# Performance work log

Measured on AMD Instinct MI355X. Metric: run time of the kernel, lower is better.

Reference implementation:

```python
import jax, jax.numpy as jnp
import numpy as np

DECAY = 0.99
EPS = 1e-06


def setup_inputs() -> dict:
    key = jax.random.key(0)
    k1, k2, k3 = jax.random.split(key, 3)
    B, S, D, K = 8, 8192, 256, 2048
    x = jax.random.normal(k1, (B, S, D), dtype=jnp.float32)
    embed = jax.random.normal(k2, (K, D), dtype=jnp.float32)
    cluster_size = jnp.ones((K,), dtype=jnp.float32)
    embed_avg = jax.random.normal(k3, (K, D), dtype=jnp.float32)
    return {"x": x, "embed": embed, "cluster_size": cluster_size, "embed_avg": embed_avg}


def reference(x, embed, cluster_size, embed_avg):
    # x: [B, S, D]; embed/embed_avg: [K, D]; cluster_size: [K]
    B, S, D = x.shape
    K = embed.shape[0]
    xf = x.reshape(-1, D)  # [N, D]
    dist = (
        jnp.sum(xf * xf, axis=1, keepdims=True)
        - 2.0 * (xf @ embed.T)
        + jnp.sum(embed * embed, axis=1)
    )
    embed_ind_flat = jnp.argmin(dist, axis=-1)  # [N]
    quantize = embed[embed_ind_flat].reshape(B, S, D)
    embed_ind = embed_ind_flat.reshape(B, S)

    # EMA updates (training branch). one_hot.sum(0) == per-code counts,
    # one_hot.T @ x == per-code feature sums; use segment_sum (no NxK one-hot).
    counts = jax.ops.segment_sum(
        jnp.ones((B * S,), dtype=jnp.float32), embed_ind_flat, num_segments=K
    )
    embed_sum = jax.ops.segment_sum(xf, embed_ind_flat, num_segments=K)  # [K, D]
    new_cluster_size = cluster_size * DECAY + (1.0 - DECAY) * counts
    new_embed_avg = embed_avg * DECAY + (1.0 - DECAY) * embed_sum
    total = new_cluster_size.sum()
    smoothed = (new_cluster_size + EPS) / (total + EPS * K) * total  # laplace smoothing
    new_embed = new_embed_avg / smoothed[:, None]
    return quantize, embed_ind, new_cluster_size, new_embed_avg, new_embed
```

## Files before the change

kernel.cpp:

```cpp
#include <hip/hip_runtime.h>
#include <hip/hip_fp16.h>
#include <float.h>

#define DECAY 0.99f
#define OMD   0.01f
#define EPSF  1e-6f

constexpr int Bb = 8, Ss = 8192, Dd = 256, Kk = 2048;
constexpr int Nn = Bb * Ss;

constexpr long OUT_QUANT = 0;
constexpr long OUT_IND   = (long)Nn * Dd;
constexpr long OUT_NCS   = OUT_IND + Nn;
constexpr long OUT_NEA   = OUT_NCS + Kk;
constexpr long OUT_NE    = OUT_NEA + (long)Kk * Dd;

constexpr long WS_COUNTS = 0;
constexpr long WS_TOTAL  = 2048;
constexpr long WS_EE     = 2112;
constexpr long WS_BIG    = 4160;
constexpr int  PARTS     = 8;
constexpr int  CODES     = 8;

typedef __attribute__((ext_vector_type(8))) short short8;
typedef __attribute__((ext_vector_type(8))) _Float16 half8;
typedef __attribute__((ext_vector_type(4))) float floatx4;

#define WINDOW 0.5f

__device__ __forceinline__ ushort f2h(float v)
{
    __half h = __float2half(v);
    return *(ushort*)&h;
}

__global__ __launch_bounds__(256) void convert_e_kernel(
    const float* __restrict__ embed, ushort* __restrict__ e_h,
    float* __restrict__ ee)
{
    int row  = blockIdx.x * 4 + (threadIdx.x >> 6);
    int lane = threadIdx.x & 63;
    long base = (long)row * Dd + lane * 4;
    float4 v = *(const float4*)&embed[base];
    float s = v.x * v.x + v.y * v.y + v.z * v.z + v.w * v.w;
    ushort4 h;
    h.x = f2h(v.x); h.y = f2h(v.y); h.z = f2h(v.z); h.w = f2h(v.w);
    *(ushort4*)&e_h[base] = h;
    #pragma unroll
    for (int off = 32; off >= 1; off >>= 1)
        s += __shfl_xor(s, off, 64);
    if (lane == 0) ee[row] = s;
}

__global__ __launch_bounds__(256) void pass1_kernel(
    const float* __restrict__ x, const ushort* __restrict__ e_h,
    const float* __restrict__ ee, float* __restrict__ ind_out,
    int* __restrict__ qbase)
{
    __shared__ __attribute__((aligned(16))) ushort as[64 * 256];
    __shared__ float redv[4][64];
    __shared__ float red2[4][64];
    __shared__ int   redi[4][64];

    const int tid  = threadIdx.x;
    const int lane = tid & 63;
    const int quad = lane >> 4;
    const int l15  = lane & 15;
    const int w    = tid >> 6;
    const long row0 = (long)blockIdx.x * 64;

    #pragma unroll
    for (int i = 0; i < 16; ++i) {
        int li = i * 256 + tid;
        int r  = li >> 6;
        int c  = (li & 63) * 4;
        float4 v = *(const float4*)&x[row0 * Dd + (long)li * 4];
        ushort4 h;
        h.x = f2h(v.x); h.y = f2h(v.y); h.z = f2h(v.z); h.w = f2h(v.w);
        int slot = (c >> 3) ^ (r & 7);
        *(ushort4*)&as[r * 256 + slot * 8 + (c & 7)] = h;
    }
    __syncthreads();

    float bestv[16], best2v[16];
    int   besti[16];
    #pragma unroll
    for (int i = 0; i < 16; ++i) { bestv[i] = FLT_MAX; best2v[i] = FLT_MAX; besti[i] = 0; }

    for (int ct = 0; ct < Kk / 256; ++ct) {
        floatx4 acc[4][4];
        #pragma unroll
        for (int rt = 0; rt < 4; ++rt)
            #pragma unroll
            for (int jt = 0; jt < 4; ++jt)
                acc[rt][jt] = (floatx4){0.f, 0.f, 0.f, 0.f};

        const int cbase = ct * 256 + w * 64 + l15;

        #pragma unroll
        for (int ks = 0; ks < 8; ++ks) {
            half8 af[4];
            #pragma unroll
            for (int rt = 0; rt < 4; ++rt) {
                int chunk = ks * 4 + quad;
                af[rt] = *(const half8*)&as[(rt * 16 + l15) * 256 +
                                            ((chunk ^ (l15 & 7)) << 3)];
            }
            #pragma unroll
            for (int jt = 0; jt < 4; ++jt) {
                const ushort* bp = &e_h[((long)(cbase + jt * 16) << 8) +
                                        ks * 32 + quad * 8];
                half8 bf = *(const half8*)bp;
                #pragma unroll
                for (int rt = 0; rt < 4; ++rt)
                    acc[rt][jt] = __builtin_amdgcn_mfma_f32_16x16x32_f16(
                        af[rt], bf, acc[rt][jt], 0, 0, 0);
            }
        }

        #pragma unroll
        for (int jt = 0; jt < 4; ++jt) {
            int c = ct * 256 + w * 64 + jt * 16 + l15;
            float eec = ee[c];
            #pragma unroll
            for (int rt = 0; rt < 4; ++rt) {
                #pragma unroll
                for (int reg = 0; reg < 4; ++reg) {
                    float s = eec - 2.0f * acc[rt][jt][reg];
                    int slot = rt * 4 + reg;
                    if (s < bestv[slot]) {
                        best2v[slot] = bestv[slot];
                        bestv[slot] = s; besti[slot] = c;
                    } else {
                        best2v[slot] = fminf(best2v[slot], s);
                    }
                }
            }
        }
    }

    #pragma unroll
    for (int slot = 0; slot < 16; ++slot) {
        float bv = bestv[slot]; int bi = besti[slot]; float b2 = best2v[slot];
        #pragma unroll
        for (int off = 8; off >= 1; off >>= 1) {
            float ov  = __shfl_xor(bv, off, 16);
            int   oi  = __shfl_xor(bi, off, 16);
            float ov2 = __shfl_xor(b2, off, 16);
            float nm2 = fminf(fminf(b2, ov2), fmaxf(bv, ov));
            if (ov < bv) { bv = ov; bi = oi; }
            b2 = nm2;
        }
        bestv[slot] = bv; besti[slot] = bi; best2v[slot] = b2;
    }

    if (l15 == 0) {
        #pragma unroll
        for (int rt = 0; rt < 4; ++rt)
            #pragma unroll
            for (int reg = 0; reg < 4; ++reg) {
                int rloc = rt * 16 + quad * 4 + reg;
                int slot = rt * 4 + reg;
                redv[w][rloc] = bestv[slot];
                red2[w][rloc] = best2v[slot];
                redi[w][rloc] = besti[slot];
            }
    }
    __syncthreads();

    if (tid < 64) {
        float v[4], s2[4]; int ix[4];
        #pragma unroll
        for (int p = 0; p < 4; ++p) {
            v[p] = redv[p][tid]; s2[p] = red2[p][tid]; ix[p] = redi[p][tid];
        }
        float m1 = v[0]; int mi = ix[0]; int arg = 0;
        #pragma unroll
        for (int p = 1; p < 4; ++p)
            if (v[p] < m1) { m1 = v[p]; mi = ix[p]; arg = p; }
        float m2 = FLT_MAX;
        #pragma unroll
        for (int p = 0; p < 4; ++p) {
            m2 = fminf(m2, s2[p]);
            if (p != arg) m2 = fminf(m2, v[p]);
        }
        long rowAbs = row0 + tid;
        ind_out[rowAbs] = (float)mi;
        if (m2 - m1 <= WINDOW) {
            int q = atomicAdd(qbase, 1);
            qbase[1 + q] = (int)rowAbs;
        }
    }
}

constexpr int RB = 8;
__global__ __launch_bounds__(256) void pass2_kernel(
    const float* __restrict__ x, const float* __restrict__ embed,
    const float* __restrict__ ee, const int* __restrict__ qbase,
    float* __restrict__ ind_out)
{
    __shared__ float xs[RB][256];
    __shared__ float sv[RB][256];
    __shared__ int   si[RB][256];
    const int tid = threadIdx.x;
    const int count = qbase[0];

    for (int q0 = blockIdx.x * RB; q0 < count; q0 += gridDim.x * RB) {
        const int nr = (count - q0 < RB) ? (count - q0) : RB;
        __syncthreads();
        for (int r = 0; r < nr; ++r)
            xs[r][tid] = x[(long)qbase[1 + q0 + r] * Dd + tid];
        __syncthreads();

        float bv[RB]; int bi[RB];
        #pragma unroll
        for (int r = 0; r < RB; ++r) { bv[r] = FLT_MAX; bi[r] = 0; }

        for (int i = 0; i < Kk / 256; ++i) {
            const int c = i * 256 + tid;
            const float4* er = (const float4*)&embed[(long)c * Dd];
            float dot[RB];
            #pragma unroll
            for (int r = 0; r < RB; ++r) dot[r] = 0.0f;
            for (int d = 0; d < Dd / 4; ++d) {
                float4 e4 = er[d];
                #pragma unroll
                for (int r = 0; r < RB; ++r) {
                    float4 x4 = *(const float4*)&xs[r][d * 4];
                    dot[r] += e4.x * x4.x + e4.y * x4.y + e4.z * x4.z + e4.w * x4.w;
                }
            }
            float eec = ee[c];
            #pragma unroll
            for (int r = 0; r < RB; ++r) {
                float s = eec - 2.0f * dot[r];
                if (s < bv[r]) { bv[r] = s; bi[r] = c; }
            }
        }

        #pragma unroll
        for (int r = 0; r < RB; ++r) { sv[r][tid] = bv[r]; si[r][tid] = bi[r]; }
        __syncthreads();
        for (int off = 128; off >= 1; off >>= 1) {
            if (tid < off) {
                #pragma unroll
                for (int r = 0; r < RB; ++r) {
                    float v2 = sv[r][tid + off]; int i2 = si[r][tid + off];
                    if (v2 < sv[r][tid] || (v2 == sv[r][tid] && i2 < si[r][tid])) {
                        sv[r][tid] = v2; si[r][tid] = i2;
                    }
                }
            }
            __syncthreads();
        }
        if (tid < nr)
            ind_out[qbase[1 + q0 + tid]] = (float)si[tid][0];
        __syncthreads();
    }
}

__global__ __launch_bounds__(256) void quant_gather_kernel(
    const float* __restrict__ embed, const float* __restrict__ ind_f,
    float* __restrict__ quant)
{
    long row  = (long)blockIdx.x * 4 + (threadIdx.x >> 6);
    int  lane = threadIdx.x & 63;
    int  idx  = (int)ind_f[row];
    float4 ev = *(const float4*)&embed[(long)idx * Dd + lane * 4];
    *(float4*)&quant[row * Dd + lane * 4] = ev;
}

template <int USE_ATOMIC>
__global__ __launch_bounds__(256) void segsum_kernel(
    const float* __restrict__ x, const float* __restrict__ ind_f,
    float* __restrict__ dst, float* __restrict__ counts)
{
    __shared__ float part[CODES][4][256];
    __shared__ float cnt_l[CODES][4];
    const int tid  = threadIdx.x;
    const int w    = tid >> 6;
    const int lane = tid & 63;
    const int k0   = (blockIdx.x >> 3) * CODES;
    const int s    = blockIdx.x & 7;

    constexpr int STRIP = Nn / PARTS;
    constexpr int WAVE_ROWS = STRIP / 4;
    const int base0 = s * STRIP + w * WAVE_ROWS;

    float4 acc[CODES];
    int    cnt[CODES];
    #pragma unroll
    for (int c = 0; c < CODES; ++c) { acc[c] = (float4){0.f,0.f,0.f,0.f}; cnt[c] = 0; }

    for (int win = 0; win < WAVE_ROWS; win += 64) {
        int idx = (int)ind_f[base0 + win + lane];
        unsigned rel = (unsigned)(idx - k0);
        unsigned long long m = __ballot(rel < (unsigned)CODES);
        while (m) {
            int l = __ffsll((unsigned long long)m) - 1;
            m &= m - 1;
            int code = __shfl((int)rel, l, 64);
            long row = base0 + win + l;
            float4 v = *(const float4*)&x[row * Dd + lane * 4];
            switch (code) {
                case 0: acc[0].x+=v.x; acc[0].y+=v.y; acc[0].z+=v.z; acc[0].w+=v.w; cnt[0]++; break;
                case 1: acc[1].x+=v.x; acc[1].y+=v.y; acc[1].z+=v.z; acc[1].w+=v.w; cnt[1]++; break;
                case 2: acc[2].x+=v.x; acc[2].y+=v.y; acc[2].z+=v.z; acc[2].w+=v.w; cnt[2]++; break;
                case 3: acc[3].x+=v.x; acc[3].y+=v.y; acc[3].z+=v.z; acc[3].w+=v.w; cnt[3]++; break;
                case 4: acc[4].x+=v.x; acc[4].y+=v.y; acc[4].z+=v.z; acc[4].w+=v.w; cnt[4]++; break;
                case 5: acc[5].x+=v.x; acc[5].y+=v.y; acc[5].z+=v.z; acc[5].w+=v.w; cnt[5]++; break;
                case 6: acc[6].x+=v.x; acc[6].y+=v.y; acc[6].z+=v.z; acc[6].w+=v.w; cnt[6]++; break;
                case 7: acc[7].x+=v.x; acc[7].y+=v.y; acc[7].z+=v.z; acc[7].w+=v.w; cnt[7]++; break;
            }
        }
    }

    #pragma unroll
    for (int c = 0; c < CODES; ++c) {
        *(float4*)&part[c][w][lane * 4] = acc[c];
        if (lane == 0) cnt_l[c][w] = (float)cnt[c];
    }
    __syncthreads();

    #pragma unroll
    for (int c = 0; c < CODES; ++c) {
        float sum = part[c][0][tid] + part[c][1][tid] + part[c][2][tid] + part[c][3][tid];
        if (USE_ATOMIC) {
            if (sum != 0.0f) atomicAdd(&dst[(long)(k0 + c) * Dd + tid], sum);
        } else {
            dst[((long)s * Kk + (k0 + c)) * Dd + tid] = sum;
        }
    }
    if (tid < CODES)
        atomicAdd(&counts[k0 + tid],
                  cnt_l[tid][0] + cnt_l[tid][1] + cnt_l[tid][2] + cnt_l[tid][3]);
}

__global__ __launch_bounds__(256) void ema_cs_kernel(
    const float* __restrict__ cs, const float* __restrict__ counts,
    float* __restrict__ ncs, float* __restrict__ total_ws)
{
    __shared__ float red[256];
    int tid = threadIdx.x;
    float s = 0.0f;
    #pragma unroll
    for (int i = 0; i < 8; ++i) {
        int k = tid + i * 256;
        float v = cs[k] * DECAY + OMD * counts[k];
        ncs[k] = v;
        s += v;
    }
    red[tid] = s;
    __syncthreads();
    #pragma unroll
    for (int off = 128; off >= 1; off >>= 1) {
        if (tid < off) red[tid] += red[tid + off];
        __syncthreads();
    }
    if (tid == 0) total_ws[0] = red[0];
}

__global__ __launch_bounds__(256) void nea_ne_kernel(
    const float* __restrict__ ea, const float* __restrict__ partials,
    int nparts, const float* __restrict__ ncs, const float* __restrict__ total_ws,
    float* __restrict__ nea, float* __restrict__ ne)
{
    long g = ((long)blockIdx.x * 256 + threadIdx.x) * 4;
    int  k = (int)(g >> 8);
    int  d = (int)(g & 255);

    float4 sv = {0.f, 0.f, 0.f, 0.f};
    for (int p = 0; p < nparts; ++p) {
        float4 pv = *(const float4*)&partials[((long)p * Kk + k) * Dd + d];
        sv.x += pv.x; sv.y += pv.y; sv.z += pv.z; sv.w += pv.w;
    }

    float4 av = *(const float4*)&ea[g];
    float4 out_nea;
    out_nea.x = av.x * DECAY + OMD * sv.x;
    out_nea.y = av.y * DECAY + OMD * sv.y;
    out_nea.z = av.z * DECAY + OMD * sv.z;
    out_nea.w = av.w * DECAY + OMD * sv.w;
    *(float4*)&nea[g] = out_nea;

    float total = total_ws[0];
    float sm = (ncs[k] + EPSF) / (total + EPSF * (float)Kk) * total;
    float inv = 1.0f / sm;
    float4 out_ne;
    out_ne.x = out_nea.x * inv;
    out_ne.y = out_nea.y * inv;
    out_ne.z = out_nea.z * inv;
    out_ne.w = out_nea.w * inv;
    *(float4*)&ne[g] = out_ne;
}

extern "C" void kernel_launch(void* const* d_in, const int* in_sizes, int n_in,
                              void* d_out, int out_size, void* d_ws, size_t ws_size,
                              hipStream_t stream)
{
    const float* x     = (const float*)d_in[0];
    const float* embed = (const float*)d_in[1];
    const float* cs    = (const float*)d_in[2];
    const float* ea    = (const float*)d_in[3];

    float* out   = (float*)d_out;
    float* quant = out + OUT_QUANT;
    float* ind_f = out + OUT_IND;
    float* ncs   = out + OUT_NCS;
    float* nea   = out + OUT_NEA;
    float* ne    = out + OUT_NE;

    float* ws     = (float*)d_ws;
    float* counts = ws + WS_COUNTS;
    float* total  = ws + WS_TOTAL;
    float* ee     = ws + WS_EE;
    float* big    = ws + WS_BIG;

    ushort* e_h = (ushort*)(out + OUT_NEA);
    int*    qb  = (int*)(out + OUT_NE);

    const size_t need_partials =
        (size_t)(WS_BIG + (long)PARTS * Kk * Dd) * sizeof(float) + 1024;
    const bool use_ws_partials = ws_size >= need_partials;

    hipMemsetAsync(counts, 0, Kk * sizeof(float), stream);
    hipMemsetAsync(qb, 0, sizeof(int), stream);
    if (!use_ws_partials)
        hipMemsetAsync(big, 0, (size_t)Kk * Dd * sizeof(float), stream);

    convert_e_kernel<<<Kk / 4, 256, 0, stream>>>(embed, e_h, ee);
    pass1_kernel<<<Nn / 64, 256, 0, stream>>>(x, e_h, ee, ind_f, qb);
    pass2_kernel<<<512, 256, 0, stream>>>(x, embed, ee, qb, ind_f);
    quant_gather_kernel<<<Nn / 4, 256, 0, stream>>>(embed, ind_f, quant);
    if (use_ws_partials)
        segsum_kernel<0><<<(Kk / CODES) * PARTS, 256, 0, stream>>>(x, ind_f, big, counts);
    else
        segsum_kernel<1><<<(Kk / CODES) * PARTS, 256, 0, stream>>>(x, ind_f, big, counts);
    ema_cs_kernel<<<1, 256, 0, stream>>>(cs, counts, ncs, total);
    nea_ne_kernel<<<(Kk * Dd / 4) / 256, 256, 0, stream>>>(
        ea, big, use_ws_partials ? PARTS : 1, ncs, total, nea, ne);
}
```

Baseline: 543.0 us.

## Fuse quantize gather into pass1/pass2 and shrink code tile per iteration

```diff
diff --git a/kernel.cpp b/kernel.cpp
--- a/kernel.cpp
+++ b/kernel.cpp
@@ -36,8 +36,9 @@
 
 __global__ __launch_bounds__(256) void convert_e_kernel(
     const float* __restrict__ embed, ushort* __restrict__ e_h,
-    float* __restrict__ ee)
-{
+    float* __restrict__ ee, int* __restrict__ qbase)
+{
+    if (blockIdx.x == 0 && threadIdx.x == 0) qbase[0] = 0;
     int row  = blockIdx.x * 4 + (threadIdx.x >> 6);
     int lane = threadIdx.x & 63;
     long base = (long)row * Dd + lane * 4;
@@ -52,9 +53,11 @@
     if (lane == 0) ee[row] = s;
 }
 
-__global__ __launch_bounds__(256) void pass1_kernel(
+__global__ __attribute__((amdgpu_waves_per_eu(2, 2))) __launch_bounds__(256)
+void pass1_kernel(
     const float* __restrict__ x, const ushort* __restrict__ e_h,
-    const float* __restrict__ ee, float* __restrict__ ind_out,
+    const float* __restrict__ embed, const float* __restrict__ ee,
+    float* __restrict__ ind_out, float* __restrict__ quant,
     int* __restrict__ qbase)
 {
     __shared__ __attribute__((aligned(16))) ushort as[64 * 256];
@@ -87,15 +90,15 @@
     #pragma unroll
     for (int i = 0; i < 16; ++i) { bestv[i] = FLT_MAX; best2v[i] = FLT_MAX; besti[i] = 0; }
 
-    for (int ct = 0; ct < Kk / 256; ++ct) {
-        floatx4 acc[4][4];
+    for (int ct = 0; ct < Kk / 128; ++ct) {
+        floatx4 acc[4][2];
         #pragma unroll
         for (int rt = 0; rt < 4; ++rt)
             #pragma unroll
-            for (int jt = 0; jt < 4; ++jt)
+            for (int jt = 0; jt < 2; ++jt)
                 acc[rt][jt] = (floatx4){0.f, 0.f, 0.f, 0.f};
 
-        const int cbase = ct * 256 + w * 64 + l15;
+        const int cbase = ct * 128 + w * 32 + l15;
 
         #pragma unroll
         for (int ks = 0; ks < 8; ++ks) {
@@ -107,7 +110,7 @@
                                             ((chunk ^ (l15 & 7)) << 3)];
             }
             #pragma unroll
-            for (int jt = 0; jt < 4; ++jt) {
+            for (int jt = 0; jt < 2; ++jt) {
                 const ushort* bp = &e_h[((long)(cbase + jt * 16) << 8) +
                                         ks * 32 + quad * 8];
                 half8 bf = *(const half8*)bp;
@@ -119,8 +122,8 @@
         }
 
         #pragma unroll
-        for (int jt = 0; jt < 4; ++jt) {
-            int c = ct * 256 + w * 64 + jt * 16 + l15;
+        for (int jt = 0; jt < 2; ++jt) {
+            int c = ct * 128 + w * 32 + jt * 16 + l15;
             float eec = ee[c];
             #pragma unroll
             for (int rt = 0; rt < 4; ++rt) {
@@ -186,10 +189,20 @@
         }
         long rowAbs = row0 + tid;
         ind_out[rowAbs] = (float)mi;
+        redi[0][tid] = mi;
         if (m2 - m1 <= WINDOW) {
             int q = atomicAdd(qbase, 1);
             qbase[1 + q] = (int)rowAbs;
         }
+    }
+    __syncthreads();
+
+    #pragma unroll
+    for (int rr = 0; rr < 16; ++rr) {
+        int row = w * 16 + rr;
+        int idx = redi[0][row];
+        float4 ev = *(const float4*)&embed[(long)idx * Dd + lane * 4];
+        *(float4*)&quant[(row0 + row) * Dd + lane * 4] = ev;
     }
 }
 
@@ -197,7 +210,7 @@
 __global__ __launch_bounds__(256) void pass2_kernel(
     const float* __restrict__ x, const float* __restrict__ embed,
     const float* __restrict__ ee, const int* __restrict__ qbase,
-    float* __restrict__ ind_out)
+    float* __restrict__ ind_out, float* __restrict__ quant)
 {
     __shared__ float xs[RB][256];
     __shared__ float sv[RB][256];
@@ -255,19 +268,13 @@
         }
         if (tid < nr)
             ind_out[qbase[1 + q0 + tid]] = (float)si[tid][0];
+        for (int r = 0; r < nr; ++r) {
+            int code = si[r][0];
+            long row = qbase[1 + q0 + r];
+            quant[row * Dd + tid] = embed[(long)code * Dd + tid];
+        }
         __syncthreads();
     }
-}
-
-__global__ __launch_bounds__(256) void quant_gather_kernel(
-    const float* __restrict__ embed, const float* __restrict__ ind_f,
-    float* __restrict__ quant)
-{
-    long row  = (long)blockIdx.x * 4 + (threadIdx.x >> 6);
-    int  lane = threadIdx.x & 63;
-    int  idx  = (int)ind_f[row];
-    float4 ev = *(const float4*)&embed[(long)idx * Dd + lane * 4];
-    *(float4*)&quant[row * Dd + lane * 4] = ev;
 }
 
 template <int USE_ATOMIC>
@@ -424,14 +431,12 @@
     const bool use_ws_partials = ws_size >= need_partials;
 
     hipMemsetAsync(counts, 0, Kk * sizeof(float), stream);
-    hipMemsetAsync(qb, 0, sizeof(int), stream);
     if (!use_ws_partials)
         hipMemsetAsync(big, 0, (size_t)Kk * Dd * sizeof(float), stream);
 
-    convert_e_kernel<<<Kk / 4, 256, 0, stream>>>(embed, e_h, ee);
-    pass1_kernel<<<Nn / 64, 256, 0, stream>>>(x, e_h, ee, ind_f, qb);
-    pass2_kernel<<<512, 256, 0, stream>>>(x, embed, ee, qb, ind_f);
-    quant_gather_kernel<<<Nn / 4, 256, 0, stream>>>(embed, ind_f, quant);
+    convert_e_kernel<<<Kk / 4, 256, 0, stream>>>(embed, e_h, ee, qb);
+    pass1_kernel<<<Nn / 64, 256, 0, stream>>>(x, e_h, embed, ee, ind_f, quant, qb);
+    pass2_kernel<<<512, 256, 0, stream>>>(x, embed, ee, qb, ind_f, quant);
     if (use_ws_partials)
         segsum_kernel<0><<<(Kk / CODES) * PARTS, 256, 0, stream>>>(x, ind_f, big, counts);
     else
```

Measured after the change: 447.6 us. 17.6% less time.
